# Kernel tuning notes

Measured on AMD Instinct MI355X. Metric: run time of the kernel, lower is better.

## Reference

```python
import jax, jax.numpy as jnp
import numpy as np

NH, NL, NP = 8, 4, 4  # heads, levels, points per head per level
SHAPES = [(100, 134), (50, 67), (25, 34), (13, 17)]  # (H, W) per level, strides 8/16/32/64


def rms_norm(x, w, eps=1e-6):
    return x * jax.lax.rsqrt(jnp.mean(x * x, axis=-1, keepdims=True) + eps) * w


def bilinear_sample(value_l, loc, H, W):
    """grid_sample(bilinear, zeros padding, align_corners=False) equivalent.
    value_l: (bs, nh, H*W, d); loc: (bs, Lq, nh, P, 2) normalized to [0,1].
    Returns (bs, Lq, nh, P, d)."""
    bs, Lq, nh, P, _ = loc.shape
    x = loc[..., 0] * W - 0.5
    y = loc[..., 1] * H - 0.5
    x0 = jnp.floor(x); y0 = jnp.floor(y)
    lx = x - x0; ly = y - y0
    x0i = x0.astype(jnp.int32); y0i = y0.astype(jnp.int32)
    out = None
    for dy, dx in ((0, 0), (0, 1), (1, 0), (1, 1)):
        wgt = (lx if dx else 1.0 - lx) * (ly if dy else 1.0 - ly)
        xi = x0i + dx; yi = y0i + dy
        valid = (xi >= 0) & (xi < W) & (yi >= 0) & (yi < H)
        idx = jnp.clip(yi, 0, H - 1) * W + jnp.clip(xi, 0, W - 1)  # (bs,Lq,nh,P)
        idx_t = idx.transpose(0, 2, 1, 3).reshape(bs, nh, Lq * P)
        g = jnp.take_along_axis(value_l, idx_t[..., None], axis=2)  # (bs,nh,Lq*P,d)
        g = g.reshape(bs, nh, Lq, P, -1).transpose(0, 2, 1, 3, 4)    # (bs,Lq,nh,P,d)
        term = g * (wgt * valid)[..., None]
        out = term if out is None else out + term
    return out


def _forward(query, query_pos, reference_points, norm_attn_w, Wv, bv, Woff, boff, Waw, baw, Wo, bo, ls_attn_g, norm_ffn_w, W1, b1, W2, b2, W3, b3, ls_ffn_g):
    bs, Lq, C = query.shape
    d = C // NH
    # --- pre-norm MSDeformAttn with identity=0 (LayerScale residual applied outside) ---
    normed = rms_norm(query, norm_attn_w)
    q = normed + query_pos  # query_pos only affects offsets/weights, not value
    value = (normed @ Wv.T + bv).reshape(bs, Lq, NH, d).transpose(0, 2, 1, 3)  # (bs,nh,Nv,d)
    off = (q @ Woff.T + boff).reshape(bs, Lq, NH, NL, NP, 2)
    aw = jax.nn.softmax((q @ Waw.T + baw).reshape(bs, Lq, NH, NL * NP), axis=-1)
    aw = aw.reshape(bs, Lq, NH, NL, NP)
    normalizer = jnp.array([[w, h] for (h, w) in SHAPES], dtype=query.dtype)  # (NL,2) = (W,H)
    loc = reference_points[:, :, None, :, None, :] + off / normalizer[None, None, None, :, None, :]
    out = jnp.zeros((bs, Lq, NH, d), query.dtype)
    start = 0
    for l, (H, W) in enumerate(SHAPES):
        v_l = jax.lax.dynamic_slice_in_dim(value, start, H * W, axis=2)
        samp = bilinear_sample(v_l, loc[:, :, :, l], H, W)  # (bs,Lq,nh,P,d)
        out = out + jnp.einsum('bqhpd,bqhp->bqhd', samp, aw[:, :, :, l])
        start += H * W
    attn_out = out.reshape(bs, Lq, C) @ Wo.T + bo
    x = query + ls_attn_g * attn_out
    # --- pre-norm SwiGLU FFN with LayerScale residual ---
    n2 = rms_norm(x, norm_ffn_w)
    h = jax.nn.silu(n2 @ W1.T + b1) * (n2 @ W2.T + b2)
    return x + ls_ffn_g * (h @ W3.T + b3)


def setup_inputs() -> dict:
    key = jax.random.key(0)
    ks = jax.random.split(key, 12)
    bs, C, dffn = 2, 256, 1024
    Lq = sum(h * w for h, w in SHAPES)  # 17821
    p = 0.02
    return {
        'query': jax.random.normal(ks[0], (bs, Lq, C), jnp.float32),
        'query_pos': jax.random.normal(ks[1], (bs, Lq, C), jnp.float32),
        'reference_points': jax.random.uniform(ks[2], (bs, Lq, NL, 2), jnp.float32),
        'spatial_shapes': jnp.array(SHAPES, jnp.int32),
        'level_start_index': jnp.array(np.cumsum([0] + [h * w for h, w in SHAPES])[:-1], jnp.int32),
        'norm_attn_w': jnp.ones((C,), jnp.float32),
        'Wv': jax.random.normal(ks[3], (C, C), jnp.float32) * p,
        'bv': jnp.zeros((C,), jnp.float32),
        'Woff': jax.random.normal(ks[4], (NH * NL * NP * 2, C), jnp.float32) * p,
        'boff': jax.random.uniform(ks[5], (NH * NL * NP * 2,), jnp.float32, -1.0, 1.0),
        'Waw': jax.random.normal(ks[6], (NH * NL * NP, C), jnp.float32) * p,
        'baw': jnp.zeros((NH * NL * NP,), jnp.float32),
        'Wo': jax.random.normal(ks[7], (C, C), jnp.float32) * p,
        'bo': jnp.zeros((C,), jnp.float32),
        'ls_attn_g': jnp.full((C,), 1e-4, jnp.float32),
        'norm_ffn_w': jnp.ones((C,), jnp.float32),
        'W1': jax.random.normal(ks[8], (dffn, C), jnp.float32) * p,
        'b1': jnp.zeros((dffn,), jnp.float32),
        'W2': jax.random.normal(ks[9], (dffn, C), jnp.float32) * p,
        'b2': jnp.zeros((dffn,), jnp.float32),
        'W3': jax.random.normal(ks[10], (C, dffn), jnp.float32) * p,
        'b3': jnp.zeros((C,), jnp.float32),
        'ls_ffn_g': jnp.full((C,), 1e-4, jnp.float32),
    }


def reference(query, query_pos, reference_points, spatial_shapes, level_start_index, norm_attn_w, Wv, bv, Woff, boff, Waw, baw, Wo, bo, ls_attn_g, norm_ffn_w, W1, b1, W2, b2, W3, b3, ls_ffn_g):
    del spatial_shapes, level_start_index  # static shapes baked into SHAPES
    return _forward(query, query_pos, reference_points, norm_attn_w, Wv, bv, Woff, boff, Waw, baw, Wo, bo, ls_attn_g, norm_ffn_w, W1, b1, W2, b2, W3, b3, ls_ffn_g)
```

## Files before the change

### kernel.cpp

```cpp
#include <hip/hip_runtime.h>
#include <hip/hip_bf16.h>
#include <cstddef>

#define LQ   17821
#define BS   2
#define MTOK (BS * LQ)
#define CDIM 256
#define NHD  8
#define DHEAD 32
#define DFFN 1024

typedef short bf16x4 __attribute__((ext_vector_type(4)));
typedef short bf16x8 __attribute__((ext_vector_type(8)));
typedef float f32x4  __attribute__((ext_vector_type(4)));
typedef float f32x2  __attribute__((ext_vector_type(2)));

__device__ __forceinline__ unsigned char fp8_enc(float f) {
#if __has_builtin(__builtin_amdgcn_cvt_pk_fp8_f32)
    return (unsigned char)(__builtin_amdgcn_cvt_pk_fp8_f32(f, f, 0, false) & 0xff);
#else
    unsigned s = (__float_as_uint(f) >> 31) << 7;
    float af = fabsf(f);
    if (af < 0.0078125f) return (unsigned char)s;
    af = fminf(af, 448.f);
    unsigned b = __float_as_uint(af);
    int e = (int)(b >> 23) - 127 + 7;
    unsigned m = (b >> 20) & 7;
    if (b & 0x80000) { m++; if (m == 8) { m = 0; e++; } }
    if (e < 1) return (unsigned char)s;
    if (e > 15) { e = 15; m = 6; }
    return (unsigned char)(s | ((unsigned)e << 3) | m);
#endif
}

__device__ __forceinline__ float fp8_dec_byte(unsigned x) {
    unsigned s = (x >> 7) & 1, e = (x >> 3) & 15, m = x & 7;
    float v = e ? __uint_as_float(((e + 120u) << 23) | (m << 20))
                : (float)m * 0.001953125f;
    return s ? -v : v;
}

template <bool HI>
__device__ __forceinline__ f32x2 fp8_dec2(unsigned d) {
#if __has_builtin(__builtin_amdgcn_cvt_pk_f32_fp8)
    return __builtin_amdgcn_cvt_pk_f32_fp8(d, HI);
#else
    f32x2 r;
    r[0] = fp8_dec_byte((d >> (HI ? 16 : 0)) & 0xff);
    r[1] = fp8_dec_byte((d >> (HI ? 24 : 8)) & 0xff);
    return r;
#endif
}

struct CastJobs {
    const float* src[7];
    __hip_bfloat16* dst[7];
    int n[7];
};

__global__ __launch_bounds__(256)
void cast_all(CastJobs j) {
    const int seg = blockIdx.y;
    const int i = blockIdx.x * 256 + threadIdx.x;
    if (i < j.n[seg]) j.dst[seg][i] = (__hip_bfloat16)j.src[seg][i];
}

__device__ __forceinline__ ushort bfpack(float f) {
    __hip_bfloat16 h = (__hip_bfloat16)f;
    return *(ushort*)&h;
}

template <bool ADD_POS>
__global__ __launch_bounds__(256)
void rmsnorm_kernel(const float* __restrict__ x, const float* __restrict__ pos,
                    const float* __restrict__ w,
                    __hip_bfloat16* __restrict__ outN, __hip_bfloat16* __restrict__ outQ) {
    const int tok = blockIdx.x * 4 + (threadIdx.x >> 6);
    if (tok >= MTOK) return;
    const int lane = threadIdx.x & 63;
    const size_t base = (size_t)tok * CDIM + lane * 4;
    const float4 v = *(const float4*)&x[base];
    float ss = v.x * v.x + v.y * v.y + v.z * v.z + v.w * v.w;
#pragma unroll
    for (int m = 1; m < 64; m <<= 1) ss += __shfl_xor(ss, m, 64);
    const float r = rsqrtf(ss * (1.0f / CDIM) + 1e-6f);
    const float4 wv = *(const float4*)&w[lane * 4];
    const float n0 = v.x * r * wv.x, n1 = v.y * r * wv.y;
    const float n2 = v.z * r * wv.z, n3 = v.w * r * wv.w;
    ushort4 o;
    o.x = bfpack(n0); o.y = bfpack(n1); o.z = bfpack(n2); o.w = bfpack(n3);
    *(ushort4*)&outN[base] = o;
    if (ADD_POS) {
        const float4 p = *(const float4*)&pos[base];
        ushort4 q;
        q.x = bfpack(n0 + p.x); q.y = bfpack(n1 + p.y);
        q.z = bfpack(n2 + p.z); q.w = bfpack(n3 + p.w);
        *(ushort4*)&outQ[base] = q;
    }
}

#define GBM 128
#define GBN 128

template <int MODE, int BKT, typename OUTT>
__global__ __launch_bounds__(256, 2)
void mfma_gemm(const __hip_bfloat16* __restrict__ A,
               const __hip_bfloat16* __restrict__ B1, const float* __restrict__ bias1,
               const __hip_bfloat16* __restrict__ B2, const float* __restrict__ bias2,
               const float* __restrict__ resid, const float* __restrict__ ls,
               OUTT* __restrict__ out, int M, int N, int K) {
    constexpr int LDKT = BKT + 8;
    constexpr int CH = BKT / 16;
    constexpr int CPR = BKT / 8;

    __shared__ short As[GBM * LDKT];
    __shared__ short Bs[GBN * LDKT];
    __shared__ short Bs2[(MODE == 3) ? GBN * LDKT : 1];

    const int tid = threadIdx.x;
    const int m0 = blockIdx.x * GBM;
    const int n0 = blockIdx.y * GBN;
    const int wave = tid >> 6;
    const int lane = tid & 63;
    const int wm = (wave >> 1) * 64;
    const int wn = (wave & 1) * 64;
    const int fr = lane & 15;
    const int fq = lane >> 4;

    f32x4 acc[4][4] = {};
    f32x4 acc2[(MODE == 3) ? 4 : 1][(MODE == 3) ? 4 : 1] = {};

    int srow[CH], skc[CH];
#pragma unroll
    for (int cc = 0; cc < CH; ++cc) {
        const int g = tid + cc * 256;
        srow[cc] = g / CPR;
        skc[cc] = (g % CPR) * 8;
    }
    const uint4 zero4 = make_uint4(0, 0, 0, 0);

    uint4 ra[CH], rb[CH], rc[(MODE == 3) ? CH : 1];
#pragma unroll
    for (int cc = 0; cc < CH; ++cc) {
        const int gm = m0 + srow[cc];
        ra[cc] = (gm < M) ? *(const uint4*)&A[(size_t)gm * K + skc[cc]] : zero4;
        rb[cc] = *(const uint4*)&B1[(size_t)(n0 + srow[cc]) * K + skc[cc]];
        if constexpr (MODE == 3)
            rc[cc] = *(const uint4*)&B2[(size_t)(n0 + srow[cc]) * K + skc[cc]];
    }

    for (int k0 = 0; k0 < K; k0 += BKT) {
        __syncthreads();
#pragma unroll
        for (int cc = 0; cc < CH; ++cc) {
            short* pa = &As[srow[cc] * LDKT + skc[cc]];
            short* pb = &Bs[srow[cc] * LDKT + skc[cc]];
            union { uint4 u; bf16x4 h[2]; } cv;
            cv.u = ra[cc]; ((bf16x4*)pa)[0] = cv.h[0]; ((bf16x4*)pa)[1] = cv.h[1];
            cv.u = rb[cc]; ((bf16x4*)pb)[0] = cv.h[0]; ((bf16x4*)pb)[1] = cv.h[1];
            if constexpr (MODE == 3) {
                short* pc = &Bs2[srow[cc] * LDKT + skc[cc]];
                cv.u = rc[cc]; ((bf16x4*)pc)[0] = cv.h[0]; ((bf16x4*)pc)[1] = cv.h[1];
            }
        }
        __syncthreads();

        if (k0 + BKT < K) {
            const int kn = k0 + BKT;
#pragma unroll
            for (int cc = 0; cc < CH; ++cc) {
                const int gm = m0 + srow[cc];
                ra[cc] = (gm < M) ? *(const uint4*)&A[(size_t)gm * K + kn + skc[cc]] : zero4;
                rb[cc] = *(const uint4*)&B1[(size_t)(n0 + srow[cc]) * K + kn + skc[cc]];
                if constexpr (MODE == 3)
                    rc[cc] = *(const uint4*)&B2[(size_t)(n0 + srow[cc]) * K + kn + skc[cc]];
            }
        }

#pragma unroll
        for (int kk = 0; kk < BKT; kk += 32) {
            const int kq = kk + fq * 8;
            bf16x8 af[4], bfr[4];
#pragma unroll
            for (int i = 0; i < 4; ++i)
                af[i] = *(const bf16x8*)&As[(wm + i * 16 + fr) * LDKT + kq];
#pragma unroll
            for (int j = 0; j < 4; ++j)
                bfr[j] = *(const bf16x8*)&Bs[(wn + j * 16 + fr) * LDKT + kq];
#pragma unroll
            for (int i = 0; i < 4; ++i)
#pragma unroll
                for (int j = 0; j < 4; ++j)
                    acc[i][j] = __builtin_amdgcn_mfma_f32_16x16x32_bf16(af[i], bfr[j], acc[i][j], 0, 0, 0);
            if constexpr (MODE == 3) {
                bf16x8 bg[4];
#pragma unroll
                for (int j = 0; j < 4; ++j)
                    bg[j] = *(const bf16x8*)&Bs2[(wn + j * 16 + fr) * LDKT + kq];
#pragma unroll
                for (int i = 0; i < 4; ++i)
#pragma unroll
                    for (int j = 0; j < 4; ++j)
                        acc2[i][j] = __builtin_amdgcn_mfma_f32_16x16x32_bf16(af[i], bg[j], acc2[i][j], 0, 0, 0);
            }
        }
    }

#pragma unroll
    for (int i = 0; i < 4; ++i) {
#pragma unroll
        for (int r = 0; r < 4; ++r) {
            const int m = m0 + wm + i * 16 + fq * 4 + r;
            if (m >= M) continue;
#pragma unroll
            for (int j = 0; j < 4; ++j) {
                const int n = n0 + wn + j * 16 + fr;
                float v;
                if constexpr (MODE == 4)
                    v = acc[i][j][r] + ((n < 256) ? bias1[n] : bias2[n - 256]);
                else
                    v = acc[i][j][r] + bias1[n];
                if constexpr (MODE == 0 || MODE == 4) {
                    out[(size_t)m * N + n] = (OUTT)v;
                } else if constexpr (MODE == 1) {
                    const int b = (m >= LQ) ? 1 : 0;
                    const int qi = m - b * LQ;
                    const int h = n >> 5;
                    const int c = n & 31;
                    ((unsigned char*)out)[((size_t)(b * NHD + h) * LQ + qi) * DHEAD + c] = fp8_enc(v);
                } else if constexpr (MODE == 2) {
                    out[(size_t)m * N + n] =
                        (OUTT)(resid[(size_t)m * N + n] + ls[n] * v);
                } else {
                    const float sig = 1.0f / (1.0f + expf(-v));
                    const float v2 = acc2[i][j][r] + bias2[n];
                    out[(size_t)m * N + n] = (OUTT)(v * sig * v2);
                }
            }
        }
    }
}

__global__ __launch_bounds__(256)
void sample_kernel(const unsigned char* __restrict__ value,
                   const ushort* __restrict__ proj,
                   const float* __restrict__ ref,
                   __hip_bfloat16* __restrict__ out) {
    __shared__ float wsm[4][NHD][16];
    __shared__ int2  sTap[4][64][9];

    const int tok0 = blockIdx.x * 4;
    const int t = threadIdx.x;

    if (t < 32) {
        const int tl = t >> 3, h = t & 7;
        const int row = tok0 + tl;
        if (row < MTOK) {
            const ushort* lg = &proj[(size_t)row * 384 + 256 + h * 16];
            float v[16];
            float mx = -3.4e38f;
#pragma unroll
            for (int i = 0; i < 16; ++i) {
                v[i] = __uint_as_float((unsigned)lg[i] << 16);
                mx = fmaxf(mx, v[i]);
            }
            float s = 0.f;
#pragma unroll
            for (int i = 0; i < 16; ++i) { v[i] = expf(v[i] - mx); s += v[i]; }
            const float inv = 1.0f / s;
#pragma unroll
            for (int i = 0; i < 16; ++i) wsm[tl][h][i] = v[i] * inv;
        }
    }
    __syncthreads();

#pragma unroll
    for (int e = t; e < 512; e += 256) {
        const int tl = e >> 7, hp = e & 127;
        const int row = tok0 + tl;
        if (row < MTOK) {
            const int h = hp >> 4, pt = hp & 15, lv = pt >> 2;
            const int Hs[4] = {100, 50, 25, 13};
            const int Ws[4] = {134, 67, 34, 17};
            const int stt[4] = {0, 13400, 16750, 17600};
            const int H = Hs[lv], W = Ws[lv];
            const float rx = ref[((size_t)row * 4 + lv) * 2 + 0];
            const float ry = ref[((size_t)row * 4 + lv) * 2 + 1];
            const float ox = __uint_as_float((unsigned)proj[(size_t)row * 384 + h * 32 + pt * 2 + 0] << 16);
            const float oy = __uint_as_float((unsigned)proj[(size_t)row * 384 + h * 32 + pt * 2 + 1] << 16);
            const float xf = rx * (float)W + ox - 0.5f;
            const float yf = ry * (float)H + oy - 0.5f;
            const float x0f = floorf(xf), y0f = floorf(yf);
            const float fx = xf - x0f, fy = yf - y0f;
            const int x0 = (int)x0f, y0 = (int)y0f;
            const float aw = wsm[tl][h][pt];
            const int b = (row >= LQ) ? 1 : 0;
            const int base = (b * NHD + h) * LQ + stt[lv];
#pragma unroll
            for (int tap = 0; tap < 4; ++tap) {
                const int dy = tap >> 1, dx = tap & 1;
                const int xi = x0 + dx, yi = y0 + dy;
                const bool valid = (xi >= 0) & (xi < W) & (yi >= 0) & (yi < H);
                const float wgt = (dx ? fx : 1.f - fx) * (dy ? fy : 1.f - fy) * aw;
                sTap[tl][pt * 4 + tap][h] = valid
                    ? make_int2((base + yi * W + xi) * DHEAD, __float_as_int(wgt))
                    : make_int2(0, 0);
            }
        }
    }
    __syncthreads();

    const int tl = t >> 6, lane = t & 63;
    const int row = tok0 + tl;
    if (row >= MTOK) return;
    const int h = lane >> 3, c0 = (lane & 7) * 4;
    const unsigned char* vb = value + c0;
    float a0 = 0.f, a1 = 0.f, a2 = 0.f, a3 = 0.f;
#pragma unroll 8
    for (int i = 0; i < 64; ++i) {
        const int2 tp = sTap[tl][i][h];
        const float w = __int_as_float(tp.y);
        const unsigned d = *(const unsigned*)(vb + (size_t)tp.x);
        const f32x2 lo = fp8_dec2<false>(d);
        const f32x2 hi = fp8_dec2<true>(d);
        a0 = fmaf(w, lo[0], a0);
        a1 = fmaf(w, lo[1], a1);
        a2 = fmaf(w, hi[0], a2);
        a3 = fmaf(w, hi[1], a3);
    }
    ushort4 o;
    o.x = bfpack(a0); o.y = bfpack(a1); o.z = bfpack(a2); o.w = bfpack(a3);
    *(ushort4*)&out[(size_t)row * 256 + h * 32 + c0] = o;
}

extern "C" void kernel_launch(void* const* d_in, const int* in_sizes, int n_in,
                              void* d_out, int out_size, void* d_ws, size_t ws_size,
                              hipStream_t stream) {
    const float* query      = (const float*)d_in[0];
    const float* query_pos  = (const float*)d_in[1];
    const float* ref        = (const float*)d_in[2];
    const float* norm_attn_w = (const float*)d_in[5];
    const float* Wv   = (const float*)d_in[6];
    const float* bv   = (const float*)d_in[7];
    const float* Woff = (const float*)d_in[8];
    const float* boff = (const float*)d_in[9];
    const float* Waw  = (const float*)d_in[10];
    const float* baw  = (const float*)d_in[11];
    const float* Wo   = (const float*)d_in[12];
    const float* bo   = (const float*)d_in[13];
    const float* ls_attn = (const float*)d_in[14];
    const float* norm_ffn_w = (const float*)d_in[15];
    const float* W1 = (const float*)d_in[16];
    const float* b1 = (const float*)d_in[17];
    const float* W2 = (const float*)d_in[18];
    const float* b2 = (const float*)d_in[19];
    const float* W3 = (const float*)d_in[20];
    const float* b3 = (const float*)d_in[21];
    const float* ls_ffn = (const float*)d_in[22];
    float* out = (float*)d_out;

    char* ws = (char*)d_ws;
    const size_t MCb = (size_t)MTOK * CDIM * 2;
    const size_t MCf = (size_t)MTOK * CDIM * 4;
    const size_t WBYTES = 2097152;

    const bool one_chunk = ws_size >= 8 * MCb + WBYTES;

    __hip_bfloat16* normed_bf  = (__hip_bfloat16*)(ws);
    __hip_bfloat16* q_bf       = (__hip_bfloat16*)(ws + MCb);
    unsigned char*  value_u8   = (unsigned char*)(ws + 2 * MCb);
    __hip_bfloat16* proj_bf    = (__hip_bfloat16*)(ws + 3 * MCb);
    __hip_bfloat16* sampled_bf = (__hip_bfloat16*)(ws);
    float*          x_f        = (float*)(ws + 2 * MCb);
    __hip_bfloat16* n2_bf      = (__hip_bfloat16*)(ws + MCb);
    __hip_bfloat16* h_bf       = (__hip_bfloat16*)(ws + 4 * MCb);
    __hip_bfloat16* wbf        = one_chunk
        ? (__hip_bfloat16*)(ws + 8 * MCb)
        : (__hip_bfloat16*)(ws + 3 * MCb + (size_t)MTOK * 384 * 4);

    __hip_bfloat16* Wv_bf    = wbf;
    __hip_bfloat16* Wproj_bf = wbf + 65536;
    __hip_bfloat16* Wo_bf    = wbf + 163840;
    __hip_bfloat16* W1_bf    = wbf + 229376;
    __hip_bfloat16* W2_bf    = wbf + 491520;
    __hip_bfloat16* W3_bf    = wbf + 753664;

    CastJobs cj;
    cj.src[0] = Wv;   cj.dst[0] = Wv_bf;            cj.n[0] = 65536;
    cj.src[1] = Woff; cj.dst[1] = Wproj_bf;         cj.n[1] = 65536;
    cj.src[2] = Waw;  cj.dst[2] = Wproj_bf + 65536; cj.n[2] = 32768;
    cj.src[3] = Wo;   cj.dst[3] = Wo_bf;            cj.n[3] = 65536;
    cj.src[4] = W1;   cj.dst[4] = W1_bf;            cj.n[4] = 262144;
    cj.src[5] = W2;   cj.dst[5] = W2_bf;            cj.n[5] = 262144;
    cj.src[6] = W3;   cj.dst[6] = W3_bf;            cj.n[6] = 262144;
    cast_all<<<dim3(1024, 7), 256, 0, stream>>>(cj);

    const int gx = (MTOK + GBM - 1) / GBM;
    const int gr = (MTOK + 3) / 4;

    rmsnorm_kernel<true><<<gr, 256, 0, stream>>>(query, query_pos, norm_attn_w, normed_bf, q_bf);
    mfma_gemm<1, 64, unsigned char><<<dim3(gx, 2), 256, 0, stream>>>(
        normed_bf, Wv_bf, bv, nullptr, nullptr, nullptr, nullptr, value_u8, MTOK, CDIM, CDIM);
    mfma_gemm<4, 64, __hip_bfloat16><<<dim3(gx, 3), 256, 0, stream>>>(
        q_bf, Wproj_bf, boff, nullptr, baw, nullptr, nullptr, proj_bf, MTOK, 384, CDIM);
    sample_kernel<<<gr, 256, 0, stream>>>(value_u8, (const ushort*)proj_bf, ref, sampled_bf);
    mfma_gemm<2, 64, float><<<dim3(gx, 2), 256, 0, stream>>>(
        sampled_bf, Wo_bf, bo, nullptr, nullptr, query, ls_attn, x_f, MTOK, CDIM, CDIM);
    rmsnorm_kernel<false><<<gr, 256, 0, stream>>>(x_f, nullptr, norm_ffn_w, n2_bf, nullptr);
    const int chunk = one_chunk ? MTOK : LQ;
    for (int ms = 0; ms < MTOK; ms += chunk) {
        const int mc = chunk;
        const int gxc = (mc + GBM - 1) / GBM;
        mfma_gemm<3, 32, __hip_bfloat16><<<dim3(gxc, DFFN / GBN), 256, 0, stream>>>(
            n2_bf + (size_t)ms * CDIM, W1_bf, b1, W2_bf, b2, nullptr, nullptr,
            h_bf, mc, DFFN, CDIM);
        mfma_gemm<2, 64, float><<<dim3(gxc, 2), 256, 0, stream>>>(
            h_bf, W3_bf, b3, nullptr, nullptr, x_f + (size_t)ms * CDIM, ls_ffn,
            out + (size_t)ms * CDIM, mc, CDIM, DFFN);
    }
}
```

Measured before the change: 407.3 us.

## Fold FFN RMSNorm into weights and row scale, split SwiGLU into dedicated kernel

```diff
diff --git a/kernel.cpp b/kernel.cpp
--- a/kernel.cpp
+++ b/kernel.cpp
@@ -55,6 +55,7 @@
 struct CastJobs {
     const float* src[7];
     __hip_bfloat16* dst[7];
+    const float* colw[7];
     int n[7];
 };
 
@@ -62,7 +63,11 @@
 void cast_all(CastJobs j) {
     const int seg = blockIdx.y;
     const int i = blockIdx.x * 256 + threadIdx.x;
-    if (i < j.n[seg]) j.dst[seg][i] = (__hip_bfloat16)j.src[seg][i];
+    if (i < j.n[seg]) {
+        float v = j.src[seg][i];
+        if (j.colw[seg]) v *= j.colw[seg][i & 255];
+        j.dst[seg][i] = (__hip_bfloat16)v;
+    }
 }
 
 __device__ __forceinline__ ushort bfpack(float f) {
@@ -99,6 +104,22 @@
     }
 }
 
+__global__ __launch_bounds__(256)
+void rowrms_kernel(const __hip_bfloat16* __restrict__ x, float* __restrict__ r) {
+    const int tok = blockIdx.x * 4 + (threadIdx.x >> 6);
+    if (tok >= MTOK) return;
+    const int lane = threadIdx.x & 63;
+    const ushort4 u = *(const ushort4*)&x[(size_t)tok * CDIM + lane * 4];
+    const float v0 = __uint_as_float((unsigned)u.x << 16);
+    const float v1 = __uint_as_float((unsigned)u.y << 16);
+    const float v2 = __uint_as_float((unsigned)u.z << 16);
+    const float v3 = __uint_as_float((unsigned)u.w << 16);
+    float ss = v0 * v0 + v1 * v1 + v2 * v2 + v3 * v3;
+#pragma unroll
+    for (int m = 1; m < 64; m <<= 1) ss += __shfl_xor(ss, m, 64);
+    if (lane == 0) r[tok] = rsqrtf(ss * (1.0f / CDIM) + 1e-6f);
+}
+
 #define GBM 128
 #define GBN 128
 
@@ -106,8 +127,9 @@
 __global__ __launch_bounds__(256, 2)
 void mfma_gemm(const __hip_bfloat16* __restrict__ A,
                const __hip_bfloat16* __restrict__ B1, const float* __restrict__ bias1,
-               const __hip_bfloat16* __restrict__ B2, const float* __restrict__ bias2,
-               const float* __restrict__ resid, const float* __restrict__ ls,
+               const float* __restrict__ bias2,
+               const float* __restrict__ resid, const __hip_bfloat16* __restrict__ residb,
+               const float* __restrict__ ls,
                OUTT* __restrict__ out, int M, int N, int K) {
     constexpr int LDKT = BKT + 8;
     constexpr int CH = BKT / 16;
@@ -115,7 +137,6 @@
 
     __shared__ short As[GBM * LDKT];
     __shared__ short Bs[GBN * LDKT];
-    __shared__ short Bs2[(MODE == 3) ? GBN * LDKT : 1];
 
     const int tid = threadIdx.x;
     const int m0 = blockIdx.x * GBM;
@@ -128,7 +149,6 @@
     const int fq = lane >> 4;
 
     f32x4 acc[4][4] = {};
-    f32x4 acc2[(MODE == 3) ? 4 : 1][(MODE == 3) ? 4 : 1] = {};
 
     int srow[CH], skc[CH];
 #pragma unroll
@@ -139,14 +159,12 @@
     }
     const uint4 zero4 = make_uint4(0, 0, 0, 0);
 
-    uint4 ra[CH], rb[CH], rc[(MODE == 3) ? CH : 1];
+    uint4 ra[CH], rb[CH];
 #pragma unroll
     for (int cc = 0; cc < CH; ++cc) {
         const int gm = m0 + srow[cc];
         ra[cc] = (gm < M) ? *(const uint4*)&A[(size_t)gm * K + skc[cc]] : zero4;
         rb[cc] = *(const uint4*)&B1[(size_t)(n0 + srow[cc]) * K + skc[cc]];
-        if constexpr (MODE == 3)
-            rc[cc] = *(const uint4*)&B2[(size_t)(n0 + srow[cc]) * K + skc[cc]];
     }
 
     for (int k0 = 0; k0 < K; k0 += BKT) {
@@ -158,10 +176,6 @@
             union { uint4 u; bf16x4 h[2]; } cv;
             cv.u = ra[cc]; ((bf16x4*)pa)[0] = cv.h[0]; ((bf16x4*)pa)[1] = cv.h[1];
             cv.u = rb[cc]; ((bf16x4*)pb)[0] = cv.h[0]; ((bf16x4*)pb)[1] = cv.h[1];
-            if constexpr (MODE == 3) {
-                short* pc = &Bs2[srow[cc] * LDKT + skc[cc]];
-                cv.u = rc[cc]; ((bf16x4*)pc)[0] = cv.h[0]; ((bf16x4*)pc)[1] = cv.h[1];
-            }
         }
         __syncthreads();
 
@@ -172,8 +186,6 @@
                 const int gm = m0 + srow[cc];
                 ra[cc] = (gm < M) ? *(const uint4*)&A[(size_t)gm * K + kn + skc[cc]] : zero4;
                 rb[cc] = *(const uint4*)&B1[(size_t)(n0 + srow[cc]) * K + kn + skc[cc]];
-                if constexpr (MODE == 3)
-                    rc[cc] = *(const uint4*)&B2[(size_t)(n0 + srow[cc]) * K + kn + skc[cc]];
             }
         }
 
@@ -192,17 +204,6 @@
 #pragma unroll
                 for (int j = 0; j < 4; ++j)
                     acc[i][j] = __builtin_amdgcn_mfma_f32_16x16x32_bf16(af[i], bfr[j], acc[i][j], 0, 0, 0);
-            if constexpr (MODE == 3) {
-                bf16x8 bg[4];
-#pragma unroll
-                for (int j = 0; j < 4; ++j)
-                    bg[j] = *(const bf16x8*)&Bs2[(wn + j * 16 + fr) * LDKT + kq];
-#pragma unroll
-                for (int i = 0; i < 4; ++i)
-#pragma unroll
-                    for (int j = 0; j < 4; ++j)
-                        acc2[i][j] = __builtin_amdgcn_mfma_f32_16x16x32_bf16(af[i], bg[j], acc2[i][j], 0, 0, 0);
-            }
         }
     }
 
@@ -232,10 +233,109 @@
                     out[(size_t)m * N + n] =
                         (OUTT)(resid[(size_t)m * N + n] + ls[n] * v);
                 } else {
-                    const float sig = 1.0f / (1.0f + expf(-v));
-                    const float v2 = acc2[i][j][r] + bias2[n];
-                    out[(size_t)m * N + n] = (OUTT)(v * sig * v2);
+                    const float rx = __uint_as_float(
+                        (unsigned)(*(const ushort*)&residb[(size_t)m * N + n]) << 16);
+                    out[(size_t)m * N + n] = (OUTT)(rx + ls[n] * v);
                 }
+            }
+        }
+    }
+}
+
+__global__ __launch_bounds__(256, 3)
+void mfma_swiglu(const __hip_bfloat16* __restrict__ A,
+                 const __hip_bfloat16* __restrict__ B1, const float* __restrict__ bias1,
+                 const __hip_bfloat16* __restrict__ B2, const float* __restrict__ bias2,
+                 const float* __restrict__ rrow,
+                 __hip_bfloat16* __restrict__ out, int M) {
+    constexpr int BKT = 32, LDKT = 40, K = CDIM, N = DFFN;
+    __shared__ short As[128 * LDKT];
+    __shared__ short Bs[64 * LDKT];
+    __shared__ short Bs2[64 * LDKT];
+
+    const int tid = threadIdx.x;
+    const int m0 = blockIdx.x * 128;
+    const int n0 = blockIdx.y * 64;
+    const int wave = tid >> 6;
+    const int lane = tid & 63;
+    const int wm = (wave >> 1) * 64;
+    const int wn = (wave & 1) * 32;
+    const int fr = lane & 15;
+    const int fq = lane >> 4;
+
+    f32x4 acc[4][2] = {};
+    f32x4 acc2[4][2] = {};
+
+    const int arow = tid >> 2;
+    const int akc = (tid & 3) * 8;
+    const uint4 zero4 = make_uint4(0, 0, 0, 0);
+
+    uint4 ra0, ra1, rb, rc;
+    {
+        const int gm0 = m0 + arow, gm1 = m0 + arow + 64;
+        ra0 = (gm0 < M) ? *(const uint4*)&A[(size_t)gm0 * K + akc] : zero4;
+        ra1 = (gm1 < M) ? *(const uint4*)&A[(size_t)gm1 * K + akc] : zero4;
+        rb = *(const uint4*)&B1[(size_t)(n0 + arow) * K + akc];
+        rc = *(const uint4*)&B2[(size_t)(n0 + arow) * K + akc];
+    }
+
+    for (int k0 = 0; k0 < K; k0 += BKT) {
+        __syncthreads();
+        {
+            union { uint4 u; bf16x4 h[2]; } cv;
+            short* pa0 = &As[arow * LDKT + akc];
+            short* pa1 = &As[(arow + 64) * LDKT + akc];
+            short* pb = &Bs[arow * LDKT + akc];
+            short* pc = &Bs2[arow * LDKT + akc];
+            cv.u = ra0; ((bf16x4*)pa0)[0] = cv.h[0]; ((bf16x4*)pa0)[1] = cv.h[1];
+            cv.u = ra1; ((bf16x4*)pa1)[0] = cv.h[0]; ((bf16x4*)pa1)[1] = cv.h[1];
+            cv.u = rb;  ((bf16x4*)pb)[0] = cv.h[0]; ((bf16x4*)pb)[1] = cv.h[1];
+            cv.u = rc;  ((bf16x4*)pc)[0] = cv.h[0]; ((bf16x4*)pc)[1] = cv.h[1];
+        }
+        __syncthreads();
+
+        if (k0 + BKT < K) {
+            const int kn = k0 + BKT + akc;
+            const int gm0 = m0 + arow, gm1 = m0 + arow + 64;
+            ra0 = (gm0 < M) ? *(const uint4*)&A[(size_t)gm0 * K + kn] : zero4;
+            ra1 = (gm1 < M) ? *(const uint4*)&A[(size_t)gm1 * K + kn] : zero4;
+            rb = *(const uint4*)&B1[(size_t)(n0 + arow) * K + kn];
+            rc = *(const uint4*)&B2[(size_t)(n0 + arow) * K + kn];
+        }
+
+        const int kq = fq * 8;
+        bf16x8 af[4], bfr[2], bg[2];
+#pragma unroll
+        for (int i = 0; i < 4; ++i)
+            af[i] = *(const bf16x8*)&As[(wm + i * 16 + fr) * LDKT + kq];
+#pragma unroll
+        for (int j = 0; j < 2; ++j) {
+            bfr[j] = *(const bf16x8*)&Bs[(wn + j * 16 + fr) * LDKT + kq];
+            bg[j] = *(const bf16x8*)&Bs2[(wn + j * 16 + fr) * LDKT + kq];
+        }
+#pragma unroll
+        for (int i = 0; i < 4; ++i)
+#pragma unroll
+            for (int j = 0; j < 2; ++j) {
+                acc[i][j] = __builtin_amdgcn_mfma_f32_16x16x32_bf16(af[i], bfr[j], acc[i][j], 0, 0, 0);
+                acc2[i][j] = __builtin_amdgcn_mfma_f32_16x16x32_bf16(af[i], bg[j], acc2[i][j], 0, 0, 0);
+            }
+    }
+
+#pragma unroll
+    for (int i = 0; i < 4; ++i) {
+#pragma unroll
+        for (int r = 0; r < 4; ++r) {
+            const int m = m0 + wm + i * 16 + fq * 4 + r;
+            if (m >= M) continue;
+            const float rm = rrow[m];
+#pragma unroll
+            for (int j = 0; j < 2; ++j) {
+                const int n = n0 + wn + j * 16 + fr;
+                const float v1 = acc[i][j][r] * rm + bias1[n];
+                const float v2 = acc2[i][j][r] * rm + bias2[n];
+                const float sig = 1.0f / (1.0f + expf(-v1));
+                out[(size_t)m * N + n] = (__hip_bfloat16)(v1 * sig * v2);
             }
         }
     }
@@ -361,22 +461,16 @@
 
     char* ws = (char*)d_ws;
     const size_t MCb = (size_t)MTOK * CDIM * 2;
-    const size_t MCf = (size_t)MTOK * CDIM * 4;
-    const size_t WBYTES = 2097152;
-
-    const bool one_chunk = ws_size >= 8 * MCb + WBYTES;
 
     __hip_bfloat16* normed_bf  = (__hip_bfloat16*)(ws);
     __hip_bfloat16* q_bf       = (__hip_bfloat16*)(ws + MCb);
     unsigned char*  value_u8   = (unsigned char*)(ws + 2 * MCb);
     __hip_bfloat16* proj_bf    = (__hip_bfloat16*)(ws + 3 * MCb);
     __hip_bfloat16* sampled_bf = (__hip_bfloat16*)(ws);
-    float*          x_f        = (float*)(ws + 2 * MCb);
-    __hip_bfloat16* n2_bf      = (__hip_bfloat16*)(ws + MCb);
-    __hip_bfloat16* h_bf       = (__hip_bfloat16*)(ws + 4 * MCb);
-    __hip_bfloat16* wbf        = one_chunk
-        ? (__hip_bfloat16*)(ws + 8 * MCb)
-        : (__hip_bfloat16*)(ws + 3 * MCb + (size_t)MTOK * 384 * 4);
+    __hip_bfloat16* x_bf       = (__hip_bfloat16*)(ws + MCb);
+    float*          r_f        = (float*)(ws + 2 * MCb);
+    __hip_bfloat16* h_bf       = (__hip_bfloat16*)(ws + 3 * MCb);
+    __hip_bfloat16* wbf        = (__hip_bfloat16*)(ws + 7 * MCb);
 
     __hip_bfloat16* Wv_bf    = wbf;
     __hip_bfloat16* Wproj_bf = wbf + 65536;
@@ -386,13 +480,13 @@
     __hip_bfloat16* W3_bf    = wbf + 753664;
 
     CastJobs cj;
-    cj.src[0] = Wv;   cj.dst[0] = Wv_bf;            cj.n[0] = 65536;
-    cj.src[1] = Woff; cj.dst[1] = Wproj_bf;         cj.n[1] = 65536;
-    cj.src[2] = Waw;  cj.dst[2] = Wproj_bf + 65536; cj.n[2] = 32768;
-    cj.src[3] = Wo;   cj.dst[3] = Wo_bf;            cj.n[3] = 65536;
-    cj.src[4] = W1;   cj.dst[4] = W1_bf;            cj.n[4] = 262144;
-    cj.src[5] = W2;   cj.dst[5] = W2_bf;            cj.n[5] = 262144;
-    cj.src[6] = W3;   cj.dst[6] = W3_bf;            cj.n[6] = 262144;
+    cj.src[0] = Wv;   cj.dst[0] = Wv_bf;            cj.colw[0] = nullptr; cj.n[0] = 65536;
+    cj.src[1] = Woff; cj.dst[1] = Wproj_bf;         cj.colw[1] = nullptr; cj.n[1] = 65536;
+    cj.src[2] = Waw;  cj.dst[2] = Wproj_bf + 65536; cj.colw[2] = nullptr; cj.n[2] = 32768;
+    cj.src[3] = Wo;   cj.dst[3] = Wo_bf;            cj.colw[3] = nullptr; cj.n[3] = 65536;
+    cj.src[4] = W1;   cj.dst[4] = W1_bf;            cj.colw[4] = norm_ffn_w; cj.n[4] = 262144;
+    cj.src[5] = W2;   cj.dst[5] = W2_bf;            cj.colw[5] = norm_ffn_w; cj.n[5] = 262144;
+    cj.src[6] = W3;   cj.dst[6] = W3_bf;            cj.colw[6] = nullptr; cj.n[6] = 262144;
     cast_all<<<dim3(1024, 7), 256, 0, stream>>>(cj);
 
     const int gx = (MTOK + GBM - 1) / GBM;
@@ -402,20 +496,13 @@
     mfma_gemm<1, 64, unsigned char><<<dim3(gx, 2), 256, 0, stream>>>(
         normed_bf, Wv_bf, bv, nullptr, nullptr, nullptr, nullptr, value_u8, MTOK, CDIM, CDIM);
     mfma_gemm<4, 64, __hip_bfloat16><<<dim3(gx, 3), 256, 0, stream>>>(
-        q_bf, Wproj_bf, boff, nullptr, baw, nullptr, nullptr, proj_bf, MTOK, 384, CDIM);
+        q_bf, Wproj_bf, boff, baw, nullptr, nullptr, nullptr, proj_bf, MTOK, 384, CDIM);
     sample_kernel<<<gr, 256, 0, stream>>>(value_u8, (const ushort*)proj_bf, ref, sampled_bf);
-    mfma_gemm<2, 64, float><<<dim3(gx, 2), 256, 0, stream>>>(
-        sampled_bf, Wo_bf, bo, nullptr, nullptr, query, ls_attn, x_f, MTOK, CDIM, CDIM);
-    rmsnorm_kernel<false><<<gr, 256, 0, stream>>>(x_f, nullptr, norm_ffn_w, n2_bf, nullptr);
-    const int chunk = one_chunk ? MTOK : LQ;
-    for (int ms = 0; ms < MTOK; ms += chunk) {
-        const int mc = chunk;
-        const int gxc = (mc + GBM - 1) / GBM;
-        mfma_gemm<3, 32, __hip_bfloat16><<<dim3(gxc, DFFN / GBN), 256, 0, stream>>>(
-            n2_bf + (size_t)ms * CDIM, W1_bf, b1, W2_bf, b2, nullptr, nullptr,
-            h_bf, mc, DFFN, CDIM);
-        mfma_gemm<2, 64, float><<<dim3(gxc, 2), 256, 0, stream>>>(
-            h_bf, W3_bf, b3, nullptr, nullptr, x_f + (size_t)ms * CDIM, ls_ffn,
-            out + (size_t)ms * CDIM, mc, CDIM, DFFN);
-    }
-}
+    mfma_gemm<2, 64, __hip_bfloat16><<<dim3(gx, 2), 256, 0, stream>>>(
+        sampled_bf, Wo_bf, bo, nullptr, query, nullptr, ls_attn, x_bf, MTOK, CDIM, CDIM);
+    rowrms_kernel<<<gr, 256, 0, stream>>>(x_bf, r_f);
+    mfma_swiglu<<<dim3(gx, DFFN / 64), 256, 0, stream>>>(
+        x_bf, W1_bf, b1, W2_bf, b2, r_f, h_bf, MTOK);
+    mfma_gemm<5, 64, float><<<dim3(gx, 2), 256, 0, stream>>>(
+        h_bf, W3_bf, b3, nullptr, nullptr, x_bf, ls_ffn, out, MTOK, CDIM, DFFN);
+}
```

After: 407.2 us. Within noise of the previous version (-0.0%).
